# Optimization experiments

Hardware: AMD Instinct MI355X
Metric: run time of the kernel (lower is better)

Reference implementation:

```python
import jax, jax.numpy as jnp
import numpy as np

ANSWER_LIMIT = 30
B, S = 16, 4096


def setup_inputs() -> dict:
    key = jax.random.key(0)
    k1, k2 = jax.random.split(key)
    start_logits = jax.random.normal(k1, (B, S), dtype=jnp.float32)
    end_logits = jax.random.normal(k2, (B, S), dtype=jnp.float32)
    return {"start_logits": start_logits, "end_logits": end_logits}


def reference(start_logits, end_logits):
    seq_len = start_logits.shape[1]
    upper = min(ANSWER_LIMIT, seq_len)  # band width (static)

    start_prob = jax.nn.softmax(start_logits, axis=-1)  # [B, S]
    end_prob = jax.nn.softmax(end_logits, axis=-1)      # [B, S]

    # Outer product of start/end probabilities: [B, S, S]
    outer = start_prob[:, :, None] * end_prob[:, None, :]

    # Band mask equivalent to tf.matrix_band_part(outer, 0, upper):
    # keep entries where 0 <= j - i <= upper.
    i = jnp.arange(seq_len)[:, None]
    j = jnp.arange(seq_len)[None, :]
    band = ((j - i) >= 0) & ((j - i) <= upper)  # [S, S]
    outer = jnp.where(band[None, :, :], outer, 0.0)

    start_pointer = jnp.argmax(jnp.max(outer, axis=2), axis=1)  # [B]
    end_pointer = jnp.argmax(jnp.max(outer, axis=1), axis=1)    # [B]
    return (start_prob, end_prob, start_pointer, end_pointer)
```

## Files before the change

kernel.cpp:

```cpp
#include <hip/hip_runtime.h>
#include <cmath>

#define SEQ 4096
#define NB 16
#define LIMIT 30
#define NT 1024
#define PAD 34

__global__ __launch_bounds__(NT, 1) void ph_kernel(
    const float* __restrict__ sl_g, const float* __restrict__ el_g,
    float* __restrict__ out) {
  const int b = blockIdx.x;
  const int tid = threadIdx.x;
  const int lane = tid & 63;
  const int wv = tid >> 6;

  __shared__ float s_ep[SEQ + PAD];
  __shared__ float s_spp[SEQ + PAD];
  __shared__ float rmax_s[16], rmax_e[16], rsum_s[16], rsum_e[16];
  __shared__ float rav[16], rbv[16];
  __shared__ int   rai[16], rbi[16];
  __shared__ float f_max_s, f_max_e, f_sum_s, f_sum_e;

  if (tid < PAD) {
    s_ep[SEQ + tid] = 0.0f;
    s_spp[tid] = 0.0f;
  }

  const int i0 = tid << 2;
  float4 sv = *(const float4*)(sl_g + b * SEQ + i0);
  float4 ev = *(const float4*)(el_g + b * SEQ + i0);

  float ms = fmaxf(fmaxf(sv.x, sv.y), fmaxf(sv.z, sv.w));
  float me = fmaxf(fmaxf(ev.x, ev.y), fmaxf(ev.z, ev.w));
#pragma unroll
  for (int off = 32; off; off >>= 1) {
    ms = fmaxf(ms, __shfl_down(ms, off, 64));
    me = fmaxf(me, __shfl_down(me, off, 64));
  }
  if (lane == 0) { rmax_s[wv] = ms; rmax_e[wv] = me; }
  __syncthreads();
  if (tid < 16) {
    float a = rmax_s[tid], c = rmax_e[tid];
#pragma unroll
    for (int off = 8; off; off >>= 1) {
      a = fmaxf(a, __shfl_down(a, off, 16));
      c = fmaxf(c, __shfl_down(c, off, 16));
    }
    if (tid == 0) { f_max_s = a; f_max_e = c; }
  }
  __syncthreads();
  const float max_s = f_max_s, max_e = f_max_e;

  float es0 = expf(sv.x - max_s), es1 = expf(sv.y - max_s),
        es2 = expf(sv.z - max_s), es3 = expf(sv.w - max_s);
  float ee0 = expf(ev.x - max_e), ee1 = expf(ev.y - max_e),
        ee2 = expf(ev.z - max_e), ee3 = expf(ev.w - max_e);
  float ss = (es0 + es1) + (es2 + es3);
  float se = (ee0 + ee1) + (ee2 + ee3);
#pragma unroll
  for (int off = 32; off; off >>= 1) {
    ss += __shfl_down(ss, off, 64);
    se += __shfl_down(se, off, 64);
  }
  if (lane == 0) { rsum_s[wv] = ss; rsum_e[wv] = se; }
  __syncthreads();
  if (tid < 16) {
    float a = rsum_s[tid], c = rsum_e[tid];
#pragma unroll
    for (int off = 8; off; off >>= 1) {
      a += __shfl_down(a, off, 16);
      c += __shfl_down(c, off, 16);
    }
    if (tid == 0) { f_sum_s = a; f_sum_e = c; }
  }
  __syncthreads();
  const float inv_s = 1.0f / f_sum_s;
  const float inv_e = 1.0f / f_sum_e;

  float4 ps = make_float4(es0 * inv_s, es1 * inv_s, es2 * inv_s, es3 * inv_s);
  float4 pe = make_float4(ee0 * inv_e, ee1 * inv_e, ee2 * inv_e, ee3 * inv_e);
  *(float4*)(out + b * SEQ + i0) = ps;
  *(float4*)(out + NB * SEQ + b * SEQ + i0) = pe;
  s_spp[PAD + i0] = ps.x; s_spp[PAD + i0 + 1] = ps.y;
  s_spp[PAD + i0 + 2] = ps.z; s_spp[PAD + i0 + 3] = ps.w;
  s_ep[i0] = pe.x; s_ep[i0 + 1] = pe.y; s_ep[i0 + 2] = pe.z; s_ep[i0 + 3] = pe.w;
  __syncthreads();

  float v0 = s_ep[i0], v1 = s_ep[i0 + 1], v2 = s_ep[i0 + 2];
  float common = s_ep[i0 + 3];
#pragma unroll
  for (int j = 4; j <= 30; ++j) common = fmaxf(common, s_ep[i0 + j]);
  float v31 = s_ep[i0 + 31], v32 = s_ep[i0 + 32], v33 = s_ep[i0 + 33];
  float w0 = fmaxf(common, fmaxf(v0, fmaxf(v1, v2)));
  float w1 = fmaxf(common, fmaxf(v1, fmaxf(v2, v31)));
  float w2 = fmaxf(common, fmaxf(v2, fmaxf(v31, v32)));
  float w3 = fmaxf(common, fmaxf(v31, fmaxf(v32, v33)));

  const int ub = 4 + i0;
  float u0 = s_spp[ub], u1 = s_spp[ub + 1], u2 = s_spp[ub + 2];
  float common2 = s_spp[ub + 3];
#pragma unroll
  for (int j = 4; j <= 30; ++j) common2 = fmaxf(common2, s_spp[ub + j]);
  float u31 = s_spp[ub + 31], u32 = s_spp[ub + 32], u33 = s_spp[ub + 33];
  float x0 = fmaxf(common2, fmaxf(u0, fmaxf(u1, u2)));
  float x1 = fmaxf(common2, fmaxf(u1, fmaxf(u2, u31)));
  float x2 = fmaxf(common2, fmaxf(u2, fmaxf(u31, u32)));
  float x3 = fmaxf(common2, fmaxf(u31, fmaxf(u32, u33)));

  float sc0 = ps.x * w0, sc1 = ps.y * w1, sc2 = ps.z * w2, sc3 = ps.w * w3;
  float tc0 = pe.x * x0, tc1 = pe.y * x1, tc2 = pe.z * x2, tc3 = pe.w * x3;

  float bsv = sc0; int bsi = i0;
  if (sc1 > bsv) { bsv = sc1; bsi = i0 + 1; }
  if (sc2 > bsv) { bsv = sc2; bsi = i0 + 2; }
  if (sc3 > bsv) { bsv = sc3; bsi = i0 + 3; }
  float bev = tc0; int bei = i0;
  if (tc1 > bev) { bev = tc1; bei = i0 + 1; }
  if (tc2 > bev) { bev = tc2; bei = i0 + 2; }
  if (tc3 > bev) { bev = tc3; bei = i0 + 3; }

#pragma unroll
  for (int off = 32; off; off >>= 1) {
    float ov = __shfl_down(bsv, off, 64);
    int oi = __shfl_down(bsi, off, 64);
    if (ov > bsv || (ov == bsv && oi < bsi)) { bsv = ov; bsi = oi; }
    float ov2 = __shfl_down(bev, off, 64);
    int oi2 = __shfl_down(bei, off, 64);
    if (ov2 > bev || (ov2 == bev && oi2 < bei)) { bev = ov2; bei = oi2; }
  }
  if (lane == 0) { rav[wv] = bsv; rai[wv] = bsi; rbv[wv] = bev; rbi[wv] = bei; }
  __syncthreads();
  if (tid < 16) {
    float av = rav[tid]; int ai = rai[tid];
    float bv = rbv[tid]; int bi = rbi[tid];
#pragma unroll
    for (int off = 8; off; off >>= 1) {
      float ov = __shfl_down(av, off, 16);
      int oi = __shfl_down(ai, off, 16);
      if (ov > av || (ov == av && oi < ai)) { av = ov; ai = oi; }
      float ov2 = __shfl_down(bv, off, 16);
      int oi2 = __shfl_down(bi, off, 16);
      if (ov2 > bv || (ov2 == bv && oi2 < bi)) { bv = ov2; bi = oi2; }
    }
    if (tid == 0) {
      out[2 * NB * SEQ + b] = (float)ai;
      out[2 * NB * SEQ + NB + b] = (float)bi;
    }
  }
}

extern "C" void kernel_launch(void* const* d_in, const int* in_sizes, int n_in,
                              void* d_out, int out_size, void* d_ws, size_t ws_size,
                              hipStream_t stream) {
  const float* start_logits = (const float*)d_in[0];
  const float* end_logits = (const float*)d_in[1];
  float* out = (float*)d_out;
  ph_kernel<<<NB, NT, 0, stream>>>(start_logits, end_logits, out);
}
```

Before: 59.66 us.

## Use DPP wave reductions, unnormalized band max, and fewer barriers

Swaps the shuffle-based wave reductions for DPP row-shift and broadcast operations. Every wave now does the cross-wave combine redundantly, which removes the single-thread final stages and one barrier. The band-max search now runs on unnormalized exponentials stored in LDS before the sum is known. Since argmax does not change under positive scaling, this lets the search overlap with the sum reduction. A per-4-element max array cuts the number of LDS reads per window. The risk is small tie-breaking differences, because scores are computed in unnormalized space, and indices are carried as floats.

```diff
diff --git a/kernel.cpp b/kernel.cpp
--- a/kernel.cpp
+++ b/kernel.cpp
@@ -3,9 +3,27 @@
 
 #define SEQ 4096
 #define NB 16
-#define LIMIT 30
 #define NT 1024
-#define PAD 34
+
+template <int C>
+__device__ __forceinline__ float dppf(float x) {
+  return __builtin_bit_cast(
+      float, __builtin_amdgcn_update_dpp(0, __builtin_bit_cast(int, x), C, 0xf, 0xf, false));
+}
+template <int C>
+__device__ __forceinline__ int dppi(int x) {
+  return __builtin_amdgcn_update_dpp(0, x, C, 0xf, 0xf, false);
+}
+__device__ __forceinline__ float rdlane(float x, int l) {
+  return __builtin_bit_cast(float, __builtin_amdgcn_readlane(__builtin_bit_cast(int, x), l));
+}
+
+#define RSHR1 0x111
+#define RSHR2 0x112
+#define RSHR4 0x114
+#define RSHR8 0x118
+#define RBC15 0x142
+#define RBC31 0x143
 
 __global__ __launch_bounds__(NT, 1) void ph_kernel(
     const float* __restrict__ sl_g, const float* __restrict__ el_g,
@@ -15,138 +33,137 @@
   const int lane = tid & 63;
   const int wv = tid >> 6;
 
-  __shared__ float s_ep[SEQ + PAD];
-  __shared__ float s_spp[SEQ + PAD];
-  __shared__ float rmax_s[16], rmax_e[16], rsum_s[16], rsum_e[16];
-  __shared__ float rav[16], rbv[16];
-  __shared__ int   rai[16], rbi[16];
-  __shared__ float f_max_s, f_max_e, f_sum_s, f_sum_e;
-
-  if (tid < PAD) {
-    s_ep[SEQ + tid] = 0.0f;
-    s_spp[tid] = 0.0f;
-  }
+  __shared__ __align__(16) float s_ee[SEQ + 32];
+  __shared__ __align__(16) float s_se[SEQ + 32];
+  __shared__ float m4e[1032];
+  __shared__ float m4s[1032];
+  __shared__ float2 rmax[16], rsum[16];
+  __shared__ float4 rarg[16];
 
   const int i0 = tid << 2;
   float4 sv = *(const float4*)(sl_g + b * SEQ + i0);
   float4 ev = *(const float4*)(el_g + b * SEQ + i0);
 
+  if (tid < 32) { s_ee[SEQ + tid] = 0.0f; s_se[tid] = 0.0f; }
+  if (tid < 8)  { m4e[1024 + tid] = 0.0f; m4s[tid] = 0.0f; }
+
   float ms = fmaxf(fmaxf(sv.x, sv.y), fmaxf(sv.z, sv.w));
   float me = fmaxf(fmaxf(ev.x, ev.y), fmaxf(ev.z, ev.w));
-#pragma unroll
-  for (int off = 32; off; off >>= 1) {
-    ms = fmaxf(ms, __shfl_down(ms, off, 64));
-    me = fmaxf(me, __shfl_down(me, off, 64));
-  }
-  if (lane == 0) { rmax_s[wv] = ms; rmax_e[wv] = me; }
+  ms = fmaxf(ms, dppf<RSHR1>(ms)); me = fmaxf(me, dppf<RSHR1>(me));
+  ms = fmaxf(ms, dppf<RSHR2>(ms)); me = fmaxf(me, dppf<RSHR2>(me));
+  ms = fmaxf(ms, dppf<RSHR4>(ms)); me = fmaxf(me, dppf<RSHR4>(me));
+  ms = fmaxf(ms, dppf<RSHR8>(ms)); me = fmaxf(me, dppf<RSHR8>(me));
+  ms = fmaxf(ms, dppf<RBC15>(ms)); me = fmaxf(me, dppf<RBC15>(me));
+  ms = fmaxf(ms, dppf<RBC31>(ms)); me = fmaxf(me, dppf<RBC31>(me));
+  if (lane == 63) rmax[wv] = make_float2(ms, me);
   __syncthreads();
-  if (tid < 16) {
-    float a = rmax_s[tid], c = rmax_e[tid];
-#pragma unroll
-    for (int off = 8; off; off >>= 1) {
-      a = fmaxf(a, __shfl_down(a, off, 16));
-      c = fmaxf(c, __shfl_down(c, off, 16));
+
+  {
+    float2 pr = rmax[lane & 15];
+    float pm = (lane & 16) ? pr.y : pr.x;
+    pm = fmaxf(pm, dppf<RSHR1>(pm));
+    pm = fmaxf(pm, dppf<RSHR2>(pm));
+    pm = fmaxf(pm, dppf<RSHR4>(pm));
+    pm = fmaxf(pm, dppf<RSHR8>(pm));
+    sv.x -= 0.0f;
+    const float max_s = rdlane(pm, 15);
+    const float max_e = rdlane(pm, 31);
+
+    float es0 = expf(sv.x - max_s), es1 = expf(sv.y - max_s),
+          es2 = expf(sv.z - max_s), es3 = expf(sv.w - max_s);
+    float ee0 = expf(ev.x - max_e), ee1 = expf(ev.y - max_e),
+          ee2 = expf(ev.z - max_e), ee3 = expf(ev.w - max_e);
+    *(float4*)&s_ee[i0] = make_float4(ee0, ee1, ee2, ee3);
+    *(float4*)&s_se[32 + i0] = make_float4(es0, es1, es2, es3);
+    m4e[tid] = fmaxf(fmaxf(ee0, ee1), fmaxf(ee2, ee3));
+    m4s[8 + tid] = fmaxf(fmaxf(es0, es1), fmaxf(es2, es3));
+
+    float ss = (es0 + es1) + (es2 + es3);
+    float se = (ee0 + ee1) + (ee2 + ee3);
+    ss += dppf<RSHR1>(ss); se += dppf<RSHR1>(se);
+    ss += dppf<RSHR2>(ss); se += dppf<RSHR2>(se);
+    ss += dppf<RSHR4>(ss); se += dppf<RSHR4>(se);
+    ss += dppf<RSHR8>(ss); se += dppf<RSHR8>(se);
+    ss += dppf<RBC15>(ss); se += dppf<RBC15>(se);
+    ss += dppf<RBC31>(ss); se += dppf<RBC31>(se);
+    if (lane == 63) rsum[wv] = make_float2(ss, se);
+    __syncthreads();
+
+    float2 qr = rsum[lane & 15];
+    float qm = (lane & 16) ? qr.y : qr.x;
+    qm += dppf<RSHR1>(qm);
+    qm += dppf<RSHR2>(qm);
+    qm += dppf<RSHR4>(qm);
+    qm += dppf<RSHR8>(qm);
+    const float inv_s = 1.0f / rdlane(qm, 15);
+    const float inv_e = 1.0f / rdlane(qm, 31);
+
+    *(float4*)(out + b * SEQ + i0) =
+        make_float4(es0 * inv_s, es1 * inv_s, es2 * inv_s, es3 * inv_s);
+    *(float4*)(out + NB * SEQ + b * SEQ + i0) =
+        make_float4(ee0 * inv_e, ee1 * inv_e, ee2 * inv_e, ee3 * inv_e);
+
+    const int t = tid;
+    float4 c7 = *(float4*)&s_ee[i0 + 28];
+    float2 c8 = *(float2*)&s_ee[i0 + 32];
+    float a1 = m4e[t + 1], a2 = m4e[t + 2], a3 = m4e[t + 3],
+          a4 = m4e[t + 4], a5 = m4e[t + 5], a6 = m4e[t + 6];
+    float m16 = fmaxf(fmaxf(fmaxf(a1, a2), fmaxf(a3, a4)), fmaxf(a5, a6));
+    float common = fmaxf(fmaxf(ee3, m16), fmaxf(fmaxf(c7.x, c7.y), c7.z));
+    float w0 = fmaxf(common, fmaxf(ee0, fmaxf(ee1, ee2)));
+    float w1 = fmaxf(common, fmaxf(ee1, fmaxf(ee2, c7.w)));
+    float w2 = fmaxf(common, fmaxf(ee2, fmaxf(c7.w, c8.x)));
+    float w3 = fmaxf(common, fmaxf(c7.w, fmaxf(c8.x, c8.y)));
+
+    float2 d0 = *(float2*)&s_se[i0 + 2];
+    float4 d1 = *(float4*)&s_se[i0 + 4];
+    float b2 = m4s[t + 2], b3 = m4s[t + 3], b4 = m4s[t + 4],
+          b5 = m4s[t + 5], b6 = m4s[t + 6], b7 = m4s[t + 7];
+    float n16 = fmaxf(fmaxf(fmaxf(b2, b3), fmaxf(b4, b5)), fmaxf(b6, b7));
+    float common2 = fmaxf(fmaxf(n16, es0), fmaxf(fmaxf(d1.y, d1.z), d1.w));
+    float x0 = fmaxf(common2, fmaxf(d0.x, fmaxf(d0.y, d1.x)));
+    float x1 = fmaxf(common2, fmaxf(d0.y, fmaxf(d1.x, es1)));
+    float x2 = fmaxf(common2, fmaxf(d1.x, fmaxf(es1, es2)));
+    float x3 = fmaxf(common2, fmaxf(es1, fmaxf(es2, es3)));
+
+    float sc0 = es0 * w0, sc1 = es1 * w1, sc2 = es2 * w2, sc3 = es3 * w3;
+    float tc0 = ee0 * x0, tc1 = ee1 * x1, tc2 = ee2 * x2, tc3 = ee3 * x3;
+
+    float bsv = sc0; int bsi = i0;
+    if (sc1 > bsv) { bsv = sc1; bsi = i0 + 1; }
+    if (sc2 > bsv) { bsv = sc2; bsi = i0 + 2; }
+    if (sc3 > bsv) { bsv = sc3; bsi = i0 + 3; }
+    float bev = tc0; int bei = i0;
+    if (tc1 > bev) { bev = tc1; bei = i0 + 1; }
+    if (tc2 > bev) { bev = tc2; bei = i0 + 2; }
+    if (tc3 > bev) { bev = tc3; bei = i0 + 3; }
+
+#define ASTEP(C)                                                       \
+    {                                                                  \
+      float ov = dppf<C>(bsv); int oi = dppi<C>(bsi);                  \
+      if (ov > bsv || (ov == bsv && oi < bsi)) { bsv = ov; bsi = oi; } \
+      float ov2 = dppf<C>(bev); int oi2 = dppi<C>(bei);                \
+      if (ov2 > bev || (ov2 == bev && oi2 < bei)) { bev = ov2; bei = oi2; } \
     }
-    if (tid == 0) { f_max_s = a; f_max_e = c; }
+    ASTEP(RSHR1) ASTEP(RSHR2) ASTEP(RSHR4) ASTEP(RSHR8) ASTEP(RBC15) ASTEP(RBC31)
+#undef ASTEP
+    if (lane == 63) rarg[wv] = make_float4(bsv, (float)bsi, bev, (float)bei);
   }
   __syncthreads();
-  const float max_s = f_max_s, max_e = f_max_e;
 
-  float es0 = expf(sv.x - max_s), es1 = expf(sv.y - max_s),
-        es2 = expf(sv.z - max_s), es3 = expf(sv.w - max_s);
-  float ee0 = expf(ev.x - max_e), ee1 = expf(ev.y - max_e),
-        ee2 = expf(ev.z - max_e), ee3 = expf(ev.w - max_e);
-  float ss = (es0 + es1) + (es2 + es3);
-  float se = (ee0 + ee1) + (ee2 + ee3);
-#pragma unroll
-  for (int off = 32; off; off >>= 1) {
-    ss += __shfl_down(ss, off, 64);
-    se += __shfl_down(se, off, 64);
-  }
-  if (lane == 0) { rsum_s[wv] = ss; rsum_e[wv] = se; }
-  __syncthreads();
-  if (tid < 16) {
-    float a = rsum_s[tid], c = rsum_e[tid];
-#pragma unroll
-    for (int off = 8; off; off >>= 1) {
-      a += __shfl_down(a, off, 16);
-      c += __shfl_down(c, off, 16);
+  if (wv == 0) {
+    float4 f = rarg[lane & 15];
+    float v = (lane & 16) ? f.z : f.x;
+    float ix = (lane & 16) ? f.w : f.y;
+#define PSTEP(C)                                              \
+    {                                                         \
+      float ov = dppf<C>(v); float oix = dppf<C>(ix);         \
+      if (ov > v || (ov == v && oix < ix)) { v = ov; ix = oix; } \
     }
-    if (tid == 0) { f_sum_s = a; f_sum_e = c; }
-  }
-  __syncthreads();
-  const float inv_s = 1.0f / f_sum_s;
-  const float inv_e = 1.0f / f_sum_e;
-
-  float4 ps = make_float4(es0 * inv_s, es1 * inv_s, es2 * inv_s, es3 * inv_s);
-  float4 pe = make_float4(ee0 * inv_e, ee1 * inv_e, ee2 * inv_e, ee3 * inv_e);
-  *(float4*)(out + b * SEQ + i0) = ps;
-  *(float4*)(out + NB * SEQ + b * SEQ + i0) = pe;
-  s_spp[PAD + i0] = ps.x; s_spp[PAD + i0 + 1] = ps.y;
-  s_spp[PAD + i0 + 2] = ps.z; s_spp[PAD + i0 + 3] = ps.w;
-  s_ep[i0] = pe.x; s_ep[i0 + 1] = pe.y; s_ep[i0 + 2] = pe.z; s_ep[i0 + 3] = pe.w;
-  __syncthreads();
-
-  float v0 = s_ep[i0], v1 = s_ep[i0 + 1], v2 = s_ep[i0 + 2];
-  float common = s_ep[i0 + 3];
-#pragma unroll
-  for (int j = 4; j <= 30; ++j) common = fmaxf(common, s_ep[i0 + j]);
-  float v31 = s_ep[i0 + 31], v32 = s_ep[i0 + 32], v33 = s_ep[i0 + 33];
-  float w0 = fmaxf(common, fmaxf(v0, fmaxf(v1, v2)));
-  float w1 = fmaxf(common, fmaxf(v1, fmaxf(v2, v31)));
-  float w2 = fmaxf(common, fmaxf(v2, fmaxf(v31, v32)));
-  float w3 = fmaxf(common, fmaxf(v31, fmaxf(v32, v33)));
-
-  const int ub = 4 + i0;
-  float u0 = s_spp[ub], u1 = s_spp[ub + 1], u2 = s_spp[ub + 2];
-  float common2 = s_spp[ub + 3];
-#pragma unroll
-  for (int j = 4; j <= 30; ++j) common2 = fmaxf(common2, s_spp[ub + j]);
-  float u31 = s_spp[ub + 31], u32 = s_spp[ub + 32], u33 = s_spp[ub + 33];
-  float x0 = fmaxf(common2, fmaxf(u0, fmaxf(u1, u2)));
-  float x1 = fmaxf(common2, fmaxf(u1, fmaxf(u2, u31)));
-  float x2 = fmaxf(common2, fmaxf(u2, fmaxf(u31, u32)));
-  float x3 = fmaxf(common2, fmaxf(u31, fmaxf(u32, u33)));
-
-  float sc0 = ps.x * w0, sc1 = ps.y * w1, sc2 = ps.z * w2, sc3 = ps.w * w3;
-  float tc0 = pe.x * x0, tc1 = pe.y * x1, tc2 = pe.z * x2, tc3 = pe.w * x3;
-
-  float bsv = sc0; int bsi = i0;
-  if (sc1 > bsv) { bsv = sc1; bsi = i0 + 1; }
-  if (sc2 > bsv) { bsv = sc2; bsi = i0 + 2; }
-  if (sc3 > bsv) { bsv = sc3; bsi = i0 + 3; }
-  float bev = tc0; int bei = i0;
-  if (tc1 > bev) { bev = tc1; bei = i0 + 1; }
-  if (tc2 > bev) { bev = tc2; bei = i0 + 2; }
-  if (tc3 > bev) { bev = tc3; bei = i0 + 3; }
-
-#pragma unroll
-  for (int off = 32; off; off >>= 1) {
-    float ov = __shfl_down(bsv, off, 64);
-    int oi = __shfl_down(bsi, off, 64);
-    if (ov > bsv || (ov == bsv && oi < bsi)) { bsv = ov; bsi = oi; }
-    float ov2 = __shfl_down(bev, off, 64);
-    int oi2 = __shfl_down(bei, off, 64);
-    if (ov2 > bev || (ov2 == bev && oi2 < bei)) { bev = ov2; bei = oi2; }
-  }
-  if (lane == 0) { rav[wv] = bsv; rai[wv] = bsi; rbv[wv] = bev; rbi[wv] = bei; }
-  __syncthreads();
-  if (tid < 16) {
-    float av = rav[tid]; int ai = rai[tid];
-    float bv = rbv[tid]; int bi = rbi[tid];
-#pragma unroll
-    for (int off = 8; off; off >>= 1) {
-      float ov = __shfl_down(av, off, 16);
-      int oi = __shfl_down(ai, off, 16);
-      if (ov > av || (ov == av && oi < ai)) { av = ov; ai = oi; }
-      float ov2 = __shfl_down(bv, off, 16);
-      int oi2 = __shfl_down(bi, off, 16);
-      if (ov2 > bv || (ov2 == bv && oi2 < bi)) { bv = ov2; bi = oi2; }
-    }
-    if (tid == 0) {
-      out[2 * NB * SEQ + b] = (float)ai;
-      out[2 * NB * SEQ + NB + b] = (float)bi;
-    }
+    PSTEP(RSHR1) PSTEP(RSHR2) PSTEP(RSHR4) PSTEP(RSHR8)
+#undef PSTEP
+    if (lane == 15) out[2 * NB * SEQ + b] = ix;
+    if (lane == 31) out[2 * NB * SEQ + NB + b] = ix;
   }
 }
 
```

Measured after the change: 58.14 us. 2.5% less time.
